# Kernel optimization log

Measured on AMD Instinct MI355X. Metric: run time of the kernel, lower is better.

The kernel has to match this reference:

```python
import jax, jax.numpy as jnp
import numpy as np

N_NODES = 50000
N_EDGES = 1500000
FEAT = 128
CUTOFF = 5.0


def setup_inputs() -> dict:
    key = jax.random.key(0)
    k_x, k_ei, k_el, k_w = jax.random.split(key, 4)
    x = jax.random.normal(k_x, (N_NODES, FEAT), dtype=jnp.float32)
    edge_index = jax.random.randint(k_ei, (2, N_EDGES), 0, N_NODES, dtype=jnp.int64)
    edge_len = jax.random.uniform(k_el, (N_EDGES,), dtype=jnp.float32) * CUTOFF
    # learned params: equivariant mix (dense linear for scalar irreps, no bias),
    # log of distance scale (init sharpness=6.0), and 1->1 filter linear.
    W_mix = jax.random.normal(k_w, (FEAT, FEAT), dtype=jnp.float32) / np.sqrt(FEAT)
    log_scale = jnp.asarray(np.log(6.0), dtype=jnp.float32)
    filter_w = jnp.asarray(0.7, dtype=jnp.float32)
    filter_b = jnp.asarray(0.1, dtype=jnp.float32)
    return {"x": x, "edge_index": edge_index, "edge_len": edge_len,
            "W_mix": W_mix, "log_scale": log_scale,
            "filter_w": filter_w, "filter_b": filter_b}


def reference(x, edge_index, edge_len, W_mix, log_scale, filter_w, filter_b):
    sender = edge_index[0]
    receiver = edge_index[1]
    n_nodes = x.shape[0]

    scale = jnp.exp(log_scale).astype(edge_len.dtype)
    decay = jnp.exp(-jnp.maximum(edge_len / (scale + 1e-6), 0.0) ** 2)  # [E]
    gate = jax.nn.sigmoid(edge_len * filter_w + filter_b)               # [E]
    weights = jnp.nan_to_num(decay * gate, nan=0.0, posinf=0.0, neginf=0.0)

    # gather-scale-scatter: messages [E, F] -> per-node sum
    messages = weights[:, None].astype(x.dtype) * x[sender]
    agg = jax.ops.segment_sum(messages, receiver, num_segments=n_nodes)
    degree = jax.ops.segment_sum(jnp.ones_like(edge_len), receiver,
                                 num_segments=n_nodes)
    agg = agg / jnp.maximum(degree, 1.0)[:, None].astype(x.dtype)

    return x + agg @ W_mix
```

## Files before the change

### kernel.cpp

```cpp
#include <hip/hip_runtime.h>
#include <math.h>

#define FEAT 128
#define BSHIFT 6
#define BNODES 64
#define CAP2 2048
#define NBUCK_MAX 1024
#define EPB 4096

__device__ __forceinline__ float edge_weight(float d, float scale, float fw, float fb) {
    float t = fmaxf(d / scale, 0.0f);
    float decay = expf(-t * t);
    float g = 1.0f / (1.0f + expf(-(d * fw + fb)));
    float w = decay * g;
    if (!isfinite(w)) w = 0.0f;
    return w;
}

__device__ __forceinline__ unsigned int bf16_rne(float f) {
    unsigned int b = __float_as_uint(f);
    return (b + 0x7FFFu + ((b >> 16) & 1u)) >> 16;
}

__device__ __forceinline__ void accum8(float acc[8], uint4 u, float w) {
    acc[0] = fmaf(w, __uint_as_float(u.x << 16), acc[0]);
    acc[1] = fmaf(w, __uint_as_float(u.x & 0xFFFF0000u), acc[1]);
    acc[2] = fmaf(w, __uint_as_float(u.y << 16), acc[2]);
    acc[3] = fmaf(w, __uint_as_float(u.y & 0xFFFF0000u), acc[3]);
    acc[4] = fmaf(w, __uint_as_float(u.z << 16), acc[4]);
    acc[5] = fmaf(w, __uint_as_float(u.z & 0xFFFF0000u), acc[5]);
    acc[6] = fmaf(w, __uint_as_float(u.w << 16), acc[6]);
    acc[7] = fmaf(w, __uint_as_float(u.w & 0xFFFF0000u), acc[7]);
}

__global__ __launch_bounds__(256) void convert_scatter_kernel(
    const float4* __restrict__ x4, uint2* __restrict__ xbf, int n4,
    const int* __restrict__ sender, const int* __restrict__ recv,
    const float* __restrict__ edge_len,
    const float* __restrict__ log_scale, const float* __restrict__ filter_w,
    const float* __restrict__ filter_b,
    int* __restrict__ gcnt, unsigned long long* __restrict__ buf,
    int E, int nbuck, int cap, int nchunk) {
    __shared__ unsigned long long recS[EPB];
    __shared__ int cnt[NBUCK_MAX];
    __shared__ int segoff[NBUCK_MAX];
    __shared__ int segcur[NBUCK_MAX];
    __shared__ int resbase[NBUCK_MAX];
    __shared__ int part[256];
    const int tid = threadIdx.x;

    if ((int)blockIdx.x >= nchunk) {
        int i = ((int)blockIdx.x - nchunk) * 256 + tid;
        if (i >= n4) return;
        float4 v = x4[i];
        uint2 o;
        o.x = (bf16_rne(v.y) << 16) | bf16_rne(v.x);
        o.y = (bf16_rne(v.w) << 16) | bf16_rne(v.z);
        xbf[i] = o;
        return;
    }

    const int c = blockIdx.x;
    for (int i = tid; i < nbuck; i += 256) cnt[i] = 0;
    __syncthreads();
    const int base = c * EPB;
    const int end = min(base + EPB, E);
    const int cntE = end - base;
    for (int e = base + tid; e < end; e += 256)
        atomicAdd(&cnt[recv[e] >> BSHIFT], 1);
    __syncthreads();

    {
        int i0 = tid * 4;
        int v0 = 0, v1 = 0, v2 = 0, v3 = 0;
        if (i0 < nbuck) {
            v0 = cnt[i0];
            v1 = (i0 + 1 < nbuck) ? cnt[i0 + 1] : 0;
            v2 = (i0 + 2 < nbuck) ? cnt[i0 + 2] : 0;
            v3 = (i0 + 3 < nbuck) ? cnt[i0 + 3] : 0;
        }
        int s = v0 + v1 + v2 + v3;
        part[tid] = s;
        __syncthreads();
        for (int d = 1; d < 256; d <<= 1) {
            int t = (tid >= d) ? part[tid - d] : 0;
            __syncthreads();
            part[tid] += t;
            __syncthreads();
        }
        int run = part[tid] - s;
        if (i0 < nbuck) {
            segoff[i0] = run; run += v0;
            if (i0 + 1 < nbuck) { segoff[i0 + 1] = run; run += v1; }
            if (i0 + 2 < nbuck) { segoff[i0 + 2] = run; run += v2; }
            if (i0 + 3 < nbuck) { segoff[i0 + 3] = run; run += v3; }
        }
    }
    for (int i = tid; i < nbuck; i += 256) {
        int cc = cnt[i];
        int b0 = cc ? atomicAdd(&gcnt[i], cc) : 0;
        resbase[i] = i * cap + b0;
        segcur[i] = segoff[i];
    }
    __syncthreads();

    float scale = expf(log_scale[0]) + 1e-6f;
    float fw = filter_w[0], fb = filter_b[0];
    for (int e = base + tid; e < end; e += 256) {
        int r = recv[e];
        int s = sender[e];
        float w = edge_weight(edge_len[e], scale, fw, fb);
        int bk = r >> BSHIFT;
        int j = atomicAdd(&segcur[bk], 1);
        recS[j] = ((unsigned long long)__float_as_uint(w) << 32)
                | (unsigned int)(s & 0xFFFF)
                | ((unsigned int)(r & (BNODES - 1)) << 16)
                | ((unsigned int)(bk & 1023) << 22);
    }
    __syncthreads();

    for (int j = tid; j < cntE; j += 256) {
        unsigned long long rec = recS[j];
        int bk = ((unsigned int)rec >> 22) & 1023;
        int pos = resbase[bk] + (j - segoff[bk]);
        if (pos < (bk + 1) * cap)
            buf[pos] = rec;
    }
}

__global__ __launch_bounds__(512) void bucket_sort_aggregate_kernel(
    const uint4* __restrict__ xbf4, const unsigned long long* __restrict__ buf,
    const int* __restrict__ gcnt, uint4* __restrict__ agg_bf4,
    int* __restrict__ deg, int N, int cap) {
    __shared__ unsigned long long recS[CAP2];
    __shared__ int cnt64[BNODES];
    __shared__ int segoff[BNODES + 1];

    const int b = blockIdx.x;
    const int n0 = b << BSHIFT;
    const int tid = threadIdx.x;
    const int lane = tid & 15;
    const int grp = tid >> 4;
    const int lo = b * cap;
    const int hi = lo + min(gcnt[b], cap);

    float acc[2][8] = {{0.f,0.f,0.f,0.f,0.f,0.f,0.f,0.f},
                       {0.f,0.f,0.f,0.f,0.f,0.f,0.f,0.f}};
    int dcnt[2] = {0, 0};

    for (int pos = lo; pos < hi; pos += CAP2) {
        int cnt = min(CAP2, hi - pos);
        if (tid < BNODES) cnt64[tid] = 0;
        __syncthreads();

        unsigned long long rec[CAP2 / 512];
        int rnk[CAP2 / 512];
        int locl[CAP2 / 512];
#pragma unroll
        for (int k = 0; k < CAP2 / 512; ++k) {
            int i = k * 512 + tid;
            rnk[k] = -1;
            if (i < cnt) {
                unsigned long long r = buf[pos + i];
                int l = ((unsigned int)r >> 16) & (BNODES - 1);
                rec[k] = r;
                locl[k] = l;
                rnk[k] = atomicAdd(&cnt64[l], 1);
            }
        }
        __syncthreads();
        if (tid == 0) {
            int run = 0;
#pragma unroll
            for (int l = 0; l < BNODES; ++l) { segoff[l] = run; run += cnt64[l]; }
            segoff[BNODES] = run;
        }
        __syncthreads();
#pragma unroll
        for (int k = 0; k < CAP2 / 512; ++k)
            if (rnk[k] >= 0) recS[segoff[locl[k]] + rnk[k]] = rec[k];
        __syncthreads();

#pragma unroll
        for (int which = 0; which < 2; ++which) {
            int l = grp + which * 32;
            int s0 = segoff[l], s1 = segoff[l + 1];
            dcnt[which] += s1 - s0;
            int i = s0;
            for (; i + 4 <= s1; i += 4) {
                unsigned long long r0 = recS[i];
                unsigned long long r1 = recS[i + 1];
                unsigned long long r2 = recS[i + 2];
                unsigned long long r3 = recS[i + 3];
                float w0 = __uint_as_float((unsigned int)(r0 >> 32));
                float w1 = __uint_as_float((unsigned int)(r1 >> 32));
                float w2 = __uint_as_float((unsigned int)(r2 >> 32));
                float w3 = __uint_as_float((unsigned int)(r3 >> 32));
                int s0i = (unsigned int)r0 & 0xFFFF;
                int s1i = (unsigned int)r1 & 0xFFFF;
                int s2i = (unsigned int)r2 & 0xFFFF;
                int s3i = (unsigned int)r3 & 0xFFFF;
                uint4 u0 = xbf4[(size_t)s0i * 16 + lane];
                uint4 u1 = xbf4[(size_t)s1i * 16 + lane];
                uint4 u2 = xbf4[(size_t)s2i * 16 + lane];
                uint4 u3 = xbf4[(size_t)s3i * 16 + lane];
                accum8(acc[which], u0, w0);
                accum8(acc[which], u1, w1);
                accum8(acc[which], u2, w2);
                accum8(acc[which], u3, w3);
            }
            for (; i < s1; ++i) {
                unsigned long long ra = recS[i];
                float wa = __uint_as_float((unsigned int)(ra >> 32));
                int sa = (unsigned int)ra & 0xFFFF;
                uint4 ua = xbf4[(size_t)sa * 16 + lane];
                accum8(acc[which], ua, wa);
            }
        }
        __syncthreads();
    }

#pragma unroll
    for (int which = 0; which < 2; ++which) {
        int n = n0 + grp + which * 32;
        if (n < N) {
            uint4 o;
            o.x = (bf16_rne(acc[which][1]) << 16) | bf16_rne(acc[which][0]);
            o.y = (bf16_rne(acc[which][3]) << 16) | bf16_rne(acc[which][2]);
            o.z = (bf16_rne(acc[which][5]) << 16) | bf16_rne(acc[which][4]);
            o.w = (bf16_rne(acc[which][7]) << 16) | bf16_rne(acc[which][6]);
            agg_bf4[(size_t)n * 16 + lane] = o;
            if (lane == 0) deg[n] = dcnt[which];
        }
    }
}

__global__ __launch_bounds__(256) void finalize_kernel(
    const float* __restrict__ x, const uint4* __restrict__ agg_bf4,
    const int* __restrict__ deg, const float* __restrict__ Wm,
    float* __restrict__ out, int N) {
    __shared__ float aggS[64 * 128];
    __shared__ float Ws[128 * 64];
    const int n0 = blockIdx.x * 64;

    for (int i = threadIdx.x; i < 64 * 16; i += 256) {
        int r = i >> 4;
        int q = i & 15;
        int n = n0 + r;
        uint4 u = make_uint4(0u, 0u, 0u, 0u);
        if (n < N) u = agg_bf4[(size_t)n * 16 + q];
        float4 f0, f1;
        f0.x = __uint_as_float(u.x << 16);
        f0.y = __uint_as_float(u.x & 0xFFFF0000u);
        f0.z = __uint_as_float(u.y << 16);
        f0.w = __uint_as_float(u.y & 0xFFFF0000u);
        f1.x = __uint_as_float(u.z << 16);
        f1.y = __uint_as_float(u.z & 0xFFFF0000u);
        f1.z = __uint_as_float(u.w << 16);
        f1.w = __uint_as_float(u.w & 0xFFFF0000u);
        int m = (r >> 2) & 7;
        ((float4*)aggS)[r * 32 + ((2 * q) ^ m)] = f0;
        ((float4*)aggS)[r * 32 + ((2 * q + 1) ^ m)] = f1;
    }

    const int tc = threadIdx.x & 15;
    const int tr = threadIdx.x >> 4;

    float invd[4];
#pragma unroll
    for (int i = 0; i < 4; ++i) {
        int n = n0 + 4 * tr + i;
        float degf = 1.0f;
        if (n < N) degf = fmaxf((float)deg[n], 1.0f);
        invd[i] = 1.0f / degf;
    }

    for (int h = 0; h < 2; ++h) {
        for (int i = threadIdx.x; i < 128 * 16; i += 256) {
            int k = i >> 4;
            int j4 = i & 15;
            ((float4*)Ws)[k * 16 + j4] = ((const float4*)Wm)[k * 32 + h * 16 + j4];
        }
        __syncthreads();

        float acc[4][4];
#pragma unroll
        for (int i = 0; i < 4; ++i)
#pragma unroll
            for (int c = 0; c < 4; ++c) acc[i][c] = 0.f;

#pragma unroll 4
        for (int k0 = 0; k0 < 128; k0 += 4) {
            float4 ar4[4];
            const int chunk = (k0 >> 2) ^ (tr & 7);
#pragma unroll
            for (int i = 0; i < 4; ++i) {
                int r = 4 * tr + i;
                ar4[i] = ((const float4*)aggS)[r * 32 + chunk];
            }
            float4 wv4[4];
#pragma unroll
            for (int kk = 0; kk < 4; ++kk)
                wv4[kk] = *(const float4*)&Ws[(k0 + kk) * 64 + tc * 4];

            float wvv[4][4];
#pragma unroll
            for (int kk = 0; kk < 4; ++kk) {
                wvv[kk][0] = wv4[kk].x; wvv[kk][1] = wv4[kk].y;
                wvv[kk][2] = wv4[kk].z; wvv[kk][3] = wv4[kk].w;
            }
#pragma unroll
            for (int i = 0; i < 4; ++i) {
                float av[4] = {ar4[i].x, ar4[i].y, ar4[i].z, ar4[i].w};
#pragma unroll
                for (int kk = 0; kk < 4; ++kk)
#pragma unroll
                    for (int c = 0; c < 4; ++c)
                        acc[i][c] = fmaf(av[kk], wvv[kk][c], acc[i][c]);
            }
        }

#pragma unroll
        for (int i = 0; i < 4; ++i) {
            int n = n0 + 4 * tr + i;
            if (n < N) {
                size_t base = (size_t)n * FEAT + h * 64 + tc * 4;
                float4 xv = *(const float4*)&x[base];
                float4 o;
                o.x = xv.x + invd[i] * acc[i][0];
                o.y = xv.y + invd[i] * acc[i][1];
                o.z = xv.z + invd[i] * acc[i][2];
                o.w = xv.w + invd[i] * acc[i][3];
                *(float4*)&out[base] = o;
            }
        }
        __syncthreads();
    }
}

__global__ __launch_bounds__(256) void scatter_fallback(
    const float4* __restrict__ x4, const int* __restrict__ sender,
    const int* __restrict__ receiver, const float* __restrict__ edge_len,
    const float* __restrict__ log_scale, const float* __restrict__ filter_w,
    const float* __restrict__ filter_b, float* __restrict__ agg,
    float* __restrict__ deg, int E) {
    int gid = blockIdx.x * 256 + threadIdx.x;
    int e = gid >> 5;
    if (e >= E) return;
    int lane = gid & 31;
    int s = sender[e];
    int r = receiver[e];
    float scale = expf(log_scale[0]) + 1e-6f;
    float w = edge_weight(edge_len[e], scale, filter_w[0], filter_b[0]);
    float4 xv = x4[s * (FEAT / 4) + lane];
    float* dst = agg + (size_t)r * FEAT + lane * 4;
    unsafeAtomicAdd(dst + 0, w * xv.x);
    unsafeAtomicAdd(dst + 1, w * xv.y);
    unsafeAtomicAdd(dst + 2, w * xv.z);
    unsafeAtomicAdd(dst + 3, w * xv.w);
    if (lane == 0) unsafeAtomicAdd(&deg[r], 1.0f);
}

__global__ __launch_bounds__(256) void finalize_fallback(
    const float* __restrict__ x, const float* __restrict__ agg,
    const float* __restrict__ deg, const float* __restrict__ Wm,
    float* __restrict__ out, int N) {
    __shared__ float Wsf[FEAT * FEAT];
    for (int i = threadIdx.x * 4; i < FEAT * FEAT; i += 256 * 4)
        *(float4*)&Wsf[i] = *(const float4*)&Wm[i];
    __syncthreads();
    int half = threadIdx.x >> 7;
    int j = threadIdx.x & (FEAT - 1);
    for (int n0 = blockIdx.x * 2; n0 < N; n0 += gridDim.x * 2) {
        int n = n0 + half;
        if (n < N) {
            const float* arow = agg + (size_t)n * FEAT;
            float acc = 0.0f;
#pragma unroll 16
            for (int k = 0; k < FEAT; ++k) acc = fmaf(arow[k], Wsf[k * FEAT + j], acc);
            float invd = 1.0f / fmaxf(deg[n], 1.0f);
            size_t idx = (size_t)n * FEAT + j;
            out[idx] = x[idx] + invd * acc;
        }
    }
}

extern "C" void kernel_launch(void* const* d_in, const int* in_sizes, int n_in,
                              void* d_out, int out_size, void* d_ws, size_t ws_size,
                              hipStream_t stream) {
    const float* x         = (const float*)d_in[0];
    const int*   ei        = (const int*)d_in[1];
    const float* edge_len  = (const float*)d_in[2];
    const float* W_mix     = (const float*)d_in[3];
    const float* log_scale = (const float*)d_in[4];
    const float* filter_w  = (const float*)d_in[5];
    const float* filter_b  = (const float*)d_in[6];
    float* out = (float*)d_out;

    const int N = in_sizes[0] / FEAT;
    const int E = in_sizes[1] / 2;
    const int* sender   = ei;
    const int* receiver = ei + E;
    const int nbuck = (N + BNODES - 1) >> BSHIFT;
    const int nchunk = (E + EPB - 1) / EPB;

    size_t xbf_bytes  = (size_t)N * FEAT * 2;
    size_t aggb_bytes = (size_t)N * FEAT * 2;
    size_t gcnt_bytes = (((size_t)nbuck * 4) + 63) & ~(size_t)63;
    size_t deg_bytes  = (((size_t)N * 4) + 63) & ~(size_t)63;

    int mean = E / nbuck + 1;
    size_t head = xbf_bytes + aggb_bytes + gcnt_bytes + deg_bytes;
    size_t avail = (ws_size > head) ? ws_size - head : 0;
    int cap = (2 * mean + 512 + 63) & ~63;
    int capmax = (int)((avail / ((size_t)nbuck * 8)) & ~(size_t)63);
    if (cap > capmax) cap = capmax;
    int sigma5 = 5 * (int)sqrtf((float)mean) + 64;
    bool ok = (N <= 65536) && (nbuck <= NBUCK_MAX) && (cap >= mean + sigma5);

    if (ok) {
        char* p = (char*)d_ws;
        uint2* xbf    = (uint2*)p;                        p += xbf_bytes;
        uint4* agg_bf = (uint4*)p;                        p += aggb_bytes;
        int* gcnt     = (int*)p;                          p += gcnt_bytes;
        int* deg      = (int*)p;                          p += deg_bytes;
        unsigned long long* buf = (unsigned long long*)p;

        (void)hipMemsetAsync(gcnt, 0, (size_t)nbuck * sizeof(int), stream);

        int n4 = N * (FEAT / 4);
        int cblocks = (n4 + 255) / 256;
        convert_scatter_kernel<<<nchunk + cblocks, 256, 0, stream>>>(
            (const float4*)x, xbf, n4, sender, receiver, edge_len,
            log_scale, filter_w, filter_b, gcnt, buf, E, nbuck, cap, nchunk);
        bucket_sort_aggregate_kernel<<<nbuck, 512, 0, stream>>>(
            (const uint4*)xbf, buf, gcnt, agg_bf, deg, N, cap);
        int fblocks = (N + 63) / 64;
        finalize_kernel<<<fblocks, 256, 0, stream>>>(
            x, (const uint4*)agg_bf, deg, W_mix, out, N);
    } else {
        float* agg = (float*)d_ws;
        float* degf = agg + (size_t)N * FEAT;
        (void)hipMemsetAsync(agg, 0, ((size_t)N * FEAT + N) * sizeof(float), stream);
        int sblocks = (E * 32 + 255) / 256;
        scatter_fallback<<<sblocks, 256, 0, stream>>>(
            (const float4*)x, sender, receiver, edge_len,
            log_scale, filter_w, filter_b, agg, degf, E);
        finalize_fallback<<<512, 256, 0, stream>>>(x, agg, degf, W_mix, out, N);
    }
}
```

Measured before the change: 216.2 us.

## Fuse dense W_mix projection and residual into the bucket aggregate kernel

```diff
diff --git a/kernel.cpp b/kernel.cpp
--- a/kernel.cpp
+++ b/kernel.cpp
@@ -128,11 +128,14 @@
     }
 }
 
-__global__ __launch_bounds__(512) void bucket_sort_aggregate_kernel(
+__global__ __launch_bounds__(512) void sort_aggregate_finalize_kernel(
     const uint4* __restrict__ xbf4, const unsigned long long* __restrict__ buf,
-    const int* __restrict__ gcnt, uint4* __restrict__ agg_bf4,
-    int* __restrict__ deg, int N, int cap) {
-    __shared__ unsigned long long recS[CAP2];
+    const int* __restrict__ gcnt, const float* __restrict__ x,
+    const float* __restrict__ Wm, float* __restrict__ out, int N, int cap) {
+    __shared__ union {
+        unsigned long long recS[CAP2];
+        float aggS[BNODES * 129];
+    } S;
     __shared__ int cnt64[BNODES];
     __shared__ int segoff[BNODES + 1];
 
@@ -178,7 +181,7 @@
         __syncthreads();
 #pragma unroll
         for (int k = 0; k < CAP2 / 512; ++k)
-            if (rnk[k] >= 0) recS[segoff[locl[k]] + rnk[k]] = rec[k];
+            if (rnk[k] >= 0) S.recS[segoff[locl[k]] + rnk[k]] = rec[k];
         __syncthreads();
 
 #pragma unroll
@@ -188,10 +191,10 @@
             dcnt[which] += s1 - s0;
             int i = s0;
             for (; i + 4 <= s1; i += 4) {
-                unsigned long long r0 = recS[i];
-                unsigned long long r1 = recS[i + 1];
-                unsigned long long r2 = recS[i + 2];
-                unsigned long long r3 = recS[i + 3];
+                unsigned long long r0 = S.recS[i];
+                unsigned long long r1 = S.recS[i + 1];
+                unsigned long long r2 = S.recS[i + 2];
+                unsigned long long r3 = S.recS[i + 3];
                 float w0 = __uint_as_float((unsigned int)(r0 >> 32));
                 float w1 = __uint_as_float((unsigned int)(r1 >> 32));
                 float w2 = __uint_as_float((unsigned int)(r2 >> 32));
@@ -210,7 +213,7 @@
                 accum8(acc[which], u3, w3);
             }
             for (; i < s1; ++i) {
-                unsigned long long ra = recS[i];
+                unsigned long long ra = S.recS[i];
                 float wa = __uint_as_float((unsigned int)(ra >> 32));
                 int sa = (unsigned int)ra & 0xFFFF;
                 uint4 ua = xbf4[(size_t)sa * 16 + lane];
@@ -222,119 +225,65 @@
 
 #pragma unroll
     for (int which = 0; which < 2; ++which) {
-        int n = n0 + grp + which * 32;
+        int l = grp + which * 32;
+        float invd = 1.0f / fmaxf((float)dcnt[which], 1.0f);
+#pragma unroll
+        for (int k = 0; k < 8; ++k)
+            S.aggS[l * 129 + lane * 8 + k] = acc[which][k] * invd;
+    }
+    __syncthreads();
+
+    {
+        const int r = tid >> 3;
+        const int jg = tid & 7;
+        const float4* W4 = (const float4*)Wm;
+        float o[16];
+#pragma unroll
+        for (int i = 0; i < 16; ++i) o[i] = 0.f;
+#pragma unroll 4
+        for (int k = 0; k < FEAT; ++k) {
+            float a = S.aggS[r * 129 + k];
+            float4 w0 = W4[k * 32 + jg * 4 + 0];
+            float4 w1 = W4[k * 32 + jg * 4 + 1];
+            float4 w2 = W4[k * 32 + jg * 4 + 2];
+            float4 w3 = W4[k * 32 + jg * 4 + 3];
+            o[0]  = fmaf(a, w0.x, o[0]);
+            o[1]  = fmaf(a, w0.y, o[1]);
+            o[2]  = fmaf(a, w0.z, o[2]);
+            o[3]  = fmaf(a, w0.w, o[3]);
+            o[4]  = fmaf(a, w1.x, o[4]);
+            o[5]  = fmaf(a, w1.y, o[5]);
+            o[6]  = fmaf(a, w1.z, o[6]);
+            o[7]  = fmaf(a, w1.w, o[7]);
+            o[8]  = fmaf(a, w2.x, o[8]);
+            o[9]  = fmaf(a, w2.y, o[9]);
+            o[10] = fmaf(a, w2.z, o[10]);
+            o[11] = fmaf(a, w2.w, o[11]);
+            o[12] = fmaf(a, w3.x, o[12]);
+            o[13] = fmaf(a, w3.y, o[13]);
+            o[14] = fmaf(a, w3.z, o[14]);
+            o[15] = fmaf(a, w3.w, o[15]);
+        }
+        int n = n0 + r;
         if (n < N) {
-            uint4 o;
-            o.x = (bf16_rne(acc[which][1]) << 16) | bf16_rne(acc[which][0]);
-            o.y = (bf16_rne(acc[which][3]) << 16) | bf16_rne(acc[which][2]);
-            o.z = (bf16_rne(acc[which][5]) << 16) | bf16_rne(acc[which][4]);
-            o.w = (bf16_rne(acc[which][7]) << 16) | bf16_rne(acc[which][6]);
-            agg_bf4[(size_t)n * 16 + lane] = o;
-            if (lane == 0) deg[n] = dcnt[which];
-        }
-    }
-}
-
-__global__ __launch_bounds__(256) void finalize_kernel(
-    const float* __restrict__ x, const uint4* __restrict__ agg_bf4,
-    const int* __restrict__ deg, const float* __restrict__ Wm,
-    float* __restrict__ out, int N) {
-    __shared__ float aggS[64 * 128];
-    __shared__ float Ws[128 * 64];
-    const int n0 = blockIdx.x * 64;
-
-    for (int i = threadIdx.x; i < 64 * 16; i += 256) {
-        int r = i >> 4;
-        int q = i & 15;
-        int n = n0 + r;
-        uint4 u = make_uint4(0u, 0u, 0u, 0u);
-        if (n < N) u = agg_bf4[(size_t)n * 16 + q];
-        float4 f0, f1;
-        f0.x = __uint_as_float(u.x << 16);
-        f0.y = __uint_as_float(u.x & 0xFFFF0000u);
-        f0.z = __uint_as_float(u.y << 16);
-        f0.w = __uint_as_float(u.y & 0xFFFF0000u);
-        f1.x = __uint_as_float(u.z << 16);
-        f1.y = __uint_as_float(u.z & 0xFFFF0000u);
-        f1.z = __uint_as_float(u.w << 16);
-        f1.w = __uint_as_float(u.w & 0xFFFF0000u);
-        int m = (r >> 2) & 7;
-        ((float4*)aggS)[r * 32 + ((2 * q) ^ m)] = f0;
-        ((float4*)aggS)[r * 32 + ((2 * q + 1) ^ m)] = f1;
-    }
-
-    const int tc = threadIdx.x & 15;
-    const int tr = threadIdx.x >> 4;
-
-    float invd[4];
-#pragma unroll
-    for (int i = 0; i < 4; ++i) {
-        int n = n0 + 4 * tr + i;
-        float degf = 1.0f;
-        if (n < N) degf = fmaxf((float)deg[n], 1.0f);
-        invd[i] = 1.0f / degf;
-    }
-
-    for (int h = 0; h < 2; ++h) {
-        for (int i = threadIdx.x; i < 128 * 16; i += 256) {
-            int k = i >> 4;
-            int j4 = i & 15;
-            ((float4*)Ws)[k * 16 + j4] = ((const float4*)Wm)[k * 32 + h * 16 + j4];
-        }
-        __syncthreads();
-
-        float acc[4][4];
-#pragma unroll
-        for (int i = 0; i < 4; ++i)
-#pragma unroll
-            for (int c = 0; c < 4; ++c) acc[i][c] = 0.f;
-
-#pragma unroll 4
-        for (int k0 = 0; k0 < 128; k0 += 4) {
-            float4 ar4[4];
-            const int chunk = (k0 >> 2) ^ (tr & 7);
-#pragma unroll
-            for (int i = 0; i < 4; ++i) {
-                int r = 4 * tr + i;
-                ar4[i] = ((const float4*)aggS)[r * 32 + chunk];
-            }
-            float4 wv4[4];
-#pragma unroll
-            for (int kk = 0; kk < 4; ++kk)
-                wv4[kk] = *(const float4*)&Ws[(k0 + kk) * 64 + tc * 4];
-
-            float wvv[4][4];
-#pragma unroll
-            for (int kk = 0; kk < 4; ++kk) {
-                wvv[kk][0] = wv4[kk].x; wvv[kk][1] = wv4[kk].y;
-                wvv[kk][2] = wv4[kk].z; wvv[kk][3] = wv4[kk].w;
-            }
-#pragma unroll
-            for (int i = 0; i < 4; ++i) {
-                float av[4] = {ar4[i].x, ar4[i].y, ar4[i].z, ar4[i].w};
-#pragma unroll
-                for (int kk = 0; kk < 4; ++kk)
-#pragma unroll
-                    for (int c = 0; c < 4; ++c)
-                        acc[i][c] = fmaf(av[kk], wvv[kk][c], acc[i][c]);
-            }
-        }
-
-#pragma unroll
-        for (int i = 0; i < 4; ++i) {
-            int n = n0 + 4 * tr + i;
-            if (n < N) {
-                size_t base = (size_t)n * FEAT + h * 64 + tc * 4;
-                float4 xv = *(const float4*)&x[base];
-                float4 o;
-                o.x = xv.x + invd[i] * acc[i][0];
-                o.y = xv.y + invd[i] * acc[i][1];
-                o.z = xv.z + invd[i] * acc[i][2];
-                o.w = xv.w + invd[i] * acc[i][3];
-                *(float4*)&out[base] = o;
-            }
-        }
-        __syncthreads();
+            size_t basei = (size_t)n * FEAT + jg * 16;
+            float4 x0 = *(const float4*)&x[basei];
+            float4 x1 = *(const float4*)&x[basei + 4];
+            float4 x2 = *(const float4*)&x[basei + 8];
+            float4 x3 = *(const float4*)&x[basei + 12];
+            float4 r0 = make_float4(x0.x + o[0],  x0.y + o[1],
+                                    x0.z + o[2],  x0.w + o[3]);
+            float4 r1 = make_float4(x1.x + o[4],  x1.y + o[5],
+                                    x1.z + o[6],  x1.w + o[7]);
+            float4 r2 = make_float4(x2.x + o[8],  x2.y + o[9],
+                                    x2.z + o[10], x2.w + o[11]);
+            float4 r3 = make_float4(x3.x + o[12], x3.y + o[13],
+                                    x3.z + o[14], x3.w + o[15]);
+            *(float4*)&out[basei]      = r0;
+            *(float4*)&out[basei + 4]  = r1;
+            *(float4*)&out[basei + 8]  = r2;
+            *(float4*)&out[basei + 12] = r3;
+        }
     }
 }
 
@@ -405,12 +354,10 @@
     const int nchunk = (E + EPB - 1) / EPB;
 
     size_t xbf_bytes  = (size_t)N * FEAT * 2;
-    size_t aggb_bytes = (size_t)N * FEAT * 2;
     size_t gcnt_bytes = (((size_t)nbuck * 4) + 63) & ~(size_t)63;
-    size_t deg_bytes  = (((size_t)N * 4) + 63) & ~(size_t)63;
 
     int mean = E / nbuck + 1;
-    size_t head = xbf_bytes + aggb_bytes + gcnt_bytes + deg_bytes;
+    size_t head = xbf_bytes + gcnt_bytes;
     size_t avail = (ws_size > head) ? ws_size - head : 0;
     int cap = (2 * mean + 512 + 63) & ~63;
     int capmax = (int)((avail / ((size_t)nbuck * 8)) & ~(size_t)63);
@@ -420,10 +367,8 @@
 
     if (ok) {
         char* p = (char*)d_ws;
-        uint2* xbf    = (uint2*)p;                        p += xbf_bytes;
-        uint4* agg_bf = (uint4*)p;                        p += aggb_bytes;
-        int* gcnt     = (int*)p;                          p += gcnt_bytes;
-        int* deg      = (int*)p;                          p += deg_bytes;
+        uint2* xbf = (uint2*)p;                           p += xbf_bytes;
+        int* gcnt  = (int*)p;                             p += gcnt_bytes;
         unsigned long long* buf = (unsigned long long*)p;
 
         (void)hipMemsetAsync(gcnt, 0, (size_t)nbuck * sizeof(int), stream);
@@ -433,11 +378,8 @@
         convert_scatter_kernel<<<nchunk + cblocks, 256, 0, stream>>>(
             (const float4*)x, xbf, n4, sender, receiver, edge_len,
             log_scale, filter_w, filter_b, gcnt, buf, E, nbuck, cap, nchunk);
-        bucket_sort_aggregate_kernel<<<nbuck, 512, 0, stream>>>(
-            (const uint4*)xbf, buf, gcnt, agg_bf, deg, N, cap);
-        int fblocks = (N + 63) / 64;
-        finalize_kernel<<<fblocks, 256, 0, stream>>>(
-            x, (const uint4*)agg_bf, deg, W_mix, out, N);
+        sort_aggregate_finalize_kernel<<<nbuck, 512, 0, stream>>>(
+            (const uint4*)xbf, buf, gcnt, x, W_mix, out, N, cap);
     } else {
         float* agg = (float*)d_ws;
         float* degf = agg + (size_t)N * FEAT;
```

After: 392.7 us. 1.82x slower.
